# Optimization experiments

Hardware: AMD Instinct MI355X
Metric: run time of the kernel (lower is better)

Reference implementation:

```python
import jax, jax.numpy as jnp
import numpy as np

N = 50000      # nodes
E = 800000     # edges
HID = 64       # hidden_dim
HEADS = 4
DH = HID // HEADS
PIN = 128      # person_in_dim
DIN = 64       # disease_in_dim
NEXP = 4       # num_experts
K = 2          # topk
L = 2          # n_layers
NEG = 0.2      # gat_neg_slope


def setup_inputs() -> dict:
    key = jax.random.key(0)
    ks = iter(jax.random.split(key, 64))
    nrm = lambda shp, s=0.05: jax.random.normal(next(ks), shp, jnp.float32) * s
    d = {}
    d["features"] = jax.random.normal(next(ks), (N, PIN), jnp.float32)
    d["node_types"] = jax.random.randint(next(ks), (N,), 0, 2)
    d["src"] = jax.random.randint(next(ks), (E,), 0, N)
    d["dst"] = jax.random.randint(next(ks), (E,), 0, N)
    d["W_person"] = nrm((PIN, HID)); d["b_person"] = jnp.zeros((HID,), jnp.float32)
    d["W_disease"] = nrm((DIN, HID)); d["b_disease"] = jnp.zeros((HID,), jnp.float32)
    d["gat_W"] = nrm((L, HID, HID)); d["gat_al"] = nrm((L, HEADS, DH)); d["gat_ar"] = nrm((L, HEADS, DH))
    d["gin_eps"] = jnp.zeros((L,), jnp.float32)
    d["gin_W1"] = nrm((L, HID, HID)); d["gin_b1"] = jnp.zeros((L, HID), jnp.float32)
    d["gin_W2"] = nrm((L, HID, HID)); d["gin_b2"] = jnp.zeros((L, HID), jnp.float32)
    for p in ("gat", "gin"):
        d[p + "_gW"] = nrm((HID, NEXP)); d[p + "_gb"] = jnp.zeros((NEXP,), jnp.float32)
        d[p + "_eW1"] = nrm((NEXP, HID, HID // 2)); d[p + "_eb1"] = jnp.zeros((NEXP, HID // 2), jnp.float32)
        d[p + "_eW2"] = nrm((NEXP, HID // 2, HID)); d[p + "_eb2"] = jnp.zeros((NEXP, HID), jnp.float32)
    d["fg_W1"] = nrm((2 * HID, HID)); d["fg_b1"] = jnp.zeros((HID,), jnp.float32)
    d["fg_W2"] = nrm((HID, HID)); d["fg_b2"] = jnp.zeros((HID,), jnp.float32)
    return d


def _edge_softmax(logits, dst):
    m = jax.ops.segment_max(logits, dst, num_segments=N)
    e = jnp.exp(logits - m[dst])
    s = jax.ops.segment_sum(e, dst, num_segments=N)
    return e / (s[dst] + 1e-9)


def _gat(h, src, dst, gat_W, gat_al, gat_ar):
    for l in range(L):
        hW = (h @ gat_W[l]).reshape(N, HEADS, DH)
        el = (hW * gat_al[l]).sum(-1)                    # [N, HEADS]
        er = (hW * gat_ar[l]).sum(-1)
        lg = jax.nn.leaky_relu(el[src] + er[dst], NEG)   # [E, HEADS]
        a = _edge_softmax(lg, dst)
        out = jax.ops.segment_sum(hW[src] * a[:, :, None], dst, num_segments=N)
        h2 = out.reshape(N, HID) + h                     # residual=True
        h = jax.nn.relu(h2) if l < L - 1 else h2
    return h


def _gin(h, src, dst, gin_eps, gin_W1, gin_b1, gin_W2, gin_b2):
    deg = jax.ops.segment_sum(jnp.ones((E,), jnp.float32), dst, num_segments=N)
    inv = 1.0 / jnp.maximum(deg, 1.0)
    for l in range(L):
        agg = jax.ops.segment_sum(h[src], dst, num_segments=N) * inv[:, None]  # 'mean' aggregator
        x = (1.0 + gin_eps[l]) * h + agg                 # learn_eps=True
        x = jax.nn.relu(x @ gin_W1[l] + gin_b1[l]) @ gin_W2[l] + gin_b2[l]     # 2-layer MLP
        h = jax.nn.relu(x) if l < L - 1 else x
    return h


def _expert(h, gW, gb, eW1, eb1, eW2, eb2):
    probs = jax.nn.softmax(h @ gW + gb, axis=-1)         # [N, NEXP]
    topv, topi = jax.lax.top_k(probs, K)
    topv = topv / topv.sum(-1, keepdims=True)
    hot = jax.nn.one_hot(topi, NEXP, dtype=h.dtype)      # [N, K, NEXP]
    w = (hot * topv[..., None]).sum(1)                   # [N, NEXP] sparse weights
    e1 = jax.nn.relu(jnp.einsum('nd,edh->neh', h, eW1) + eb1)
    e2 = jnp.einsum('neh,ehd->ned', e1, eW2) + eb2       # [N, NEXP, HID]
    out = (e2 * w[:, :, None]).sum(1)
    f = hot.sum(1).mean(0)                               # routed fraction per expert
    P = probs.mean(0)
    aux = NEXP * jnp.sum(f * P)                          # switch-style load balancing
    return out, aux


def reference(features, node_types, src, dst, W_person, b_person, W_disease, b_disease,
              gat_W, gat_al, gat_ar, gin_eps, gin_W1, gin_b1, gin_W2, gin_b2,
              gat_gW, gat_gb, gat_eW1, gat_eb1, gat_eW2, gat_eb2,
              gin_gW, gin_gb, gin_eW1, gin_eb1, gin_eW2, gin_eb2,
              fg_W1, fg_b1, fg_W2, fg_b2):
    # per-type projection + scatter into shared buffer
    hp = features[:, :PIN] @ W_person + b_person
    hd = features[:, :DIN] @ W_disease + b_disease
    h = jnp.where((node_types == 0)[:, None], hp, hd)
    z_gat = _gat(h, src, dst, gat_W, gat_al, gat_ar)
    z_gin = _gin(h, src, dst, gin_eps, gin_W1, gin_b1, gin_W2, gin_b2)
    zg, aux_g = _expert(z_gat, gat_gW, gat_gb, gat_eW1, gat_eb1, gat_eW2, gat_eb2)
    zi, aux_i = _expert(z_gin, gin_gW, gin_gb, gin_eW1, gin_eb1, gin_eW2, gin_eb2)
    z = zi * zg
    u = jnp.concatenate([zg, zi], axis=-1)
    gate = jax.nn.sigmoid(jax.nn.relu(u @ fg_W1 + fg_b1) @ fg_W2 + fg_b2)
    u_prime = gate  # source calls fusion_gate(u) twice -> identical deterministic value
    z = gate * z + (1.0 - gate) * u_prime
    return z, aux_i + aux_g
```

## Files before the change

### kernel.cpp

```cpp
#include <hip/hip_runtime.h>

#define NN 50000
#define EE 800000
#define NEG 0.2f
#define NBG 391
#define NBT 392
#define NBKT 391
#define EPB 4096
#define NSEG 196

typedef __attribute__((ext_vector_type(8))) short s8;
typedef __attribute__((ext_vector_type(4))) float f4;

__device__ __forceinline__ float leaky(float x) { return x > 0.f ? x : NEG * x; }
__device__ __forceinline__ unsigned bf16r(float x) {
    unsigned u = __float_as_uint(x);
    return (u + 0x7fffu + ((u >> 16) & 1u)) >> 16;
}
__device__ __forceinline__ float lo16(unsigned p) { return __uint_as_float(p << 16); }
__device__ __forceinline__ float hi16(unsigned p) { return __uint_as_float(p & 0xffff0000u); }

__device__ __forceinline__ s8 a_from_f32(const float* p) {
    float4 u = *reinterpret_cast<const float4*>(p);
    float4 v = *reinterpret_cast<const float4*>(p + 4);
    s8 r;
    r[0] = (short)bf16r(u.x); r[1] = (short)bf16r(u.y);
    r[2] = (short)bf16r(u.z); r[3] = (short)bf16r(u.w);
    r[4] = (short)bf16r(v.x); r[5] = (short)bf16r(v.y);
    r[6] = (short)bf16r(v.z); r[7] = (short)bf16r(v.w);
    return r;
}

__global__ __launch_bounds__(256) void k_binA_pre(
        const int* __restrict__ src, const int* __restrict__ dst,
        int* __restrict__ seg_off, int* __restrict__ seg_cnt,
        unsigned* __restrict__ gseg, int* __restrict__ bucket_tot,
        const float* __restrict__ feat, const int* __restrict__ types,
        const float* __restrict__ Wp, const float* __restrict__ bp,
        const float* __restrict__ Wd, const float* __restrict__ bd,
        const float* __restrict__ gW, const float* __restrict__ al,
        const float* __restrict__ ar,
        float* __restrict__ h0f, unsigned* __restrict__ P,
        float* __restrict__ el, float* __restrict__ er) {
    __shared__ unsigned short WpT[64 * 136];
    __shared__ unsigned short WdT[64 * 72];
    __shared__ unsigned short WgT[64 * 72];
    __shared__ unsigned short y0s[4][16 * 72];
    if (blockIdx.x < NSEG) {
        unsigned* sbuf = (unsigned*)WpT;
        int* cnt = (int*)WdT;
        int* pre = (int*)WgT;
        int* ssc = (int*)y0s;
        for (int i = threadIdx.x; i < NBKT; i += 256) cnt[i] = 0;
        __syncthreads();
        int e0 = blockIdx.x * EPB;
        int nE = EE - e0; if (nE > EPB) nE = EPB;
        int b[16]; unsigned val[16]; int rk[16];
        #pragma unroll
        for (int i = 0; i < 16; i++) {
            int li = i * 256 + threadIdx.x;
            if (li < nE) {
                int e = e0 + li;
                int d = dst[e], s = src[e];
                b[i] = d >> 7;
                val[i] = ((unsigned)s << 7) | (unsigned)(d & 127);
                rk[i] = atomicAdd(&cnt[b[i]], 1);
            } else b[i] = -1;
        }
        __syncthreads();
        int t = threadIdx.x;
        int c0 = (2 * t     < NBKT) ? cnt[2 * t]     : 0;
        int c1 = (2 * t + 1 < NBKT) ? cnt[2 * t + 1] : 0;
        ssc[t] = c0 + c1;
        __syncthreads();
        for (int off = 1; off < 256; off <<= 1) {
            int u = (t >= off) ? ssc[t - off] : 0;
            __syncthreads();
            ssc[t] += u;
            __syncthreads();
        }
        int base = ssc[t] - (c0 + c1);
        pre[2 * t] = base;
        pre[2 * t + 1] = base + c0;
        __syncthreads();
        #pragma unroll
        for (int i = 0; i < 16; i++)
            if (b[i] >= 0) sbuf[pre[b[i]] + rk[i]] = val[i];
        for (int i = t; i < NBKT; i += 256) {
            seg_off[blockIdx.x * NBKT + i] = pre[i];
            seg_cnt[blockIdx.x * NBKT + i] = cnt[i];
            atomicAdd(&bucket_tot[i], cnt[i]);
        }
        __syncthreads();
        for (int i = t; i < nE; i += 256)
            gseg[(size_t)blockIdx.x * EPB + i] = sbuf[i];
        return;
    }
    for (int idx = threadIdx.x; idx < 128 * 64; idx += 256) {
        int k = idx >> 6, n = idx & 63;
        WpT[n * 136 + k] = (unsigned short)bf16r(Wp[idx]);
    }
    for (int idx = threadIdx.x; idx < 64 * 64; idx += 256) {
        int k = idx >> 6, n = idx & 63;
        WdT[n * 72 + k] = (unsigned short)bf16r(Wd[idx]);
        WgT[n * 72 + k] = (unsigned short)bf16r(gW[idx]);
    }
    __syncthreads();
    int wv = threadIdx.x >> 6, lane = threadIdx.x & 63;
    int quad = lane >> 4, l16 = lane & 15;
    int gw2 = (blockIdx.x - NSEG) * 4 + wv;
    int mtEnd = gw2 * 2 + 2; if (mtEnd > 3125) mtEnd = 3125;
    for (int mt = gw2 * 2; mt < mtEnd; mt++) {
        int row0 = mt * 16;
        const float* arow = feat + (size_t)(row0 + l16) * 128;
        f4 accp[4], accd[4];
        #pragma unroll
        for (int t = 0; t < 4; t++) { accp[t] = f4{0.f,0.f,0.f,0.f}; accd[t] = f4{0.f,0.f,0.f,0.f}; }
        #pragma unroll
        for (int ks = 0; ks < 4; ks++) {
            s8 a = a_from_f32(arow + ks * 32 + quad * 8);
            #pragma unroll
            for (int t = 0; t < 4; t++) {
                s8 b = *(const s8*)&WpT[(t * 16 + l16) * 136 + ks * 32 + quad * 8];
                accp[t] = __builtin_amdgcn_mfma_f32_16x16x32_bf16(a, b, accp[t], 0, 0, 0);
                if (ks < 2) {
                    s8 bd_ = *(const s8*)&WdT[(t * 16 + l16) * 72 + ks * 32 + quad * 8];
                    accd[t] = __builtin_amdgcn_mfma_f32_16x16x32_bf16(a, bd_, accd[t], 0, 0, 0);
                }
            }
        }
        int ty[4];
        #pragma unroll
        for (int r = 0; r < 4; r++) ty[r] = types[row0 + quad * 4 + r];
        float vv[4][4];
        #pragma unroll
        for (int t = 0; t < 4; t++) {
            int col = t * 16 + l16;
            float bpv = bp[col], bdv = bd[col];
            #pragma unroll
            for (int r = 0; r < 4; r++) {
                float v = ty[r] ? (accd[t][r] + bdv) : (accp[t][r] + bpv);
                vv[t][r] = v;
                h0f[(size_t)(row0 + quad * 4 + r) * 64 + col] = v;
                y0s[wv][(quad * 4 + r) * 72 + col] = (unsigned short)bf16r(v);
            }
        }
        s8 a0 = *(const s8*)&y0s[wv][l16 * 72 + quad * 8];
        s8 a1 = *(const s8*)&y0s[wv][l16 * 72 + 32 + quad * 8];
        f4 hw[4];
        #pragma unroll
        for (int t = 0; t < 4; t++) {
            hw[t] = f4{0.f,0.f,0.f,0.f};
            s8 b0 = *(const s8*)&WgT[(t * 16 + l16) * 72 + quad * 8];
            hw[t] = __builtin_amdgcn_mfma_f32_16x16x32_bf16(a0, b0, hw[t], 0, 0, 0);
            s8 b1_ = *(const s8*)&WgT[(t * 16 + l16) * 72 + 32 + quad * 8];
            hw[t] = __builtin_amdgcn_mfma_f32_16x16x32_bf16(a1, b1_, hw[t], 0, 0, 0);
        }
        #pragma unroll
        for (int t = 0; t < 4; t++) {
            int col = t * 16 + l16;
            float alv = al[col], arv = ar[col];
            #pragma unroll
            for (int r = 0; r < 4; r++) {
                int row = row0 + quad * 4 + r;
                float h = hw[t][r];
                P[(size_t)row * 64 + col] = bf16r(h) | (bf16r(vv[t][r]) << 16);
                float pl = h * alv, pr = h * arv;
                #pragma unroll
                for (int m = 1; m < 16; m <<= 1) {
                    pl += __shfl_xor(pl, m, 64);
                    pr += __shfl_xor(pr, m, 64);
                }
                if (l16 == 0) {
                    el[(size_t)row * 4 + t] = pl;
                    er[(size_t)row * 4 + t] = pr;
                }
            }
        }
    }
}

__global__ __launch_bounds__(256) void k_binB(
        int* __restrict__ row_start, const int* __restrict__ seg_off,
        const int* __restrict__ seg_cnt, const unsigned* __restrict__ gseg,
        int* __restrict__ csr_src, const int* __restrict__ bucket_tot) {
    __shared__ int spre[256];
    __shared__ int soff[NSEG];
    __shared__ int ss[256];
    __shared__ int kur[128];
    __shared__ int sred[4];
    int b = blockIdx.x;
    int t = threadIdx.x;
    int bt = 0;
    for (int i = t; i < b; i += 256) bt += bucket_tot[i];
    #pragma unroll
    for (int o2 = 1; o2 < 64; o2 <<= 1) bt += __shfl_xor(bt, o2, 64);
    if ((t & 63) == 0) sred[t >> 6] = bt;
    int c0 = (t < NSEG) ? seg_cnt[t * NBKT + b] : 0;
    if (t < NSEG) soff[t] = seg_off[t * NBKT + b];
    ss[t] = c0;
    __syncthreads();
    int bstart = sred[0] + sred[1] + sred[2] + sred[3];
    for (int off = 1; off < 256; off <<= 1) {
        int u = (t >= off) ? ss[t - off] : 0;
        __syncthreads();
        ss[t] += u;
        __syncthreads();
    }
    spre[t] = ss[t] - c0;
    int cntb = ss[255];
    if (t < 128) kur[t] = 0;
    __syncthreads();
    for (int idx = t; idx < cntb; idx += 256) {
        int lo = 0, hi = 255;
        #pragma unroll
        for (int s = 0; s < 8; s++) {
            int mid = (lo + hi + 1) >> 1;
            if (spre[mid] <= idx) lo = mid; else hi = mid - 1;
        }
        unsigned v = gseg[(size_t)lo * EPB + soff[lo] + (idx - spre[lo])];
        atomicAdd(&kur[v & 127], 1);
    }
    __syncthreads();
    int deg = (t < 128) ? kur[t] : 0;
    ss[t] = deg;
    __syncthreads();
    for (int off = 1; off < 256; off <<= 1) {
        int u = (t >= off) ? ss[t - off] : 0;
        __syncthreads();
        ss[t] += u;
        __syncthreads();
    }
    if (t < 128) {
        int cur = bstart + ss[t] - deg;
        kur[t] = cur;
        int d = (b << 7) + t;
        if (d < NN) row_start[d] = cur;
    }
    if (b == 0 && t == 0) row_start[NN] = EE;
    __syncthreads();
    for (int idx = t; idx < cntb; idx += 256) {
        int lo = 0, hi = 255;
        #pragma unroll
        for (int s = 0; s < 8; s++) {
            int mid = (lo + hi + 1) >> 1;
            if (spre[mid] <= idx) lo = mid; else hi = mid - 1;
        }
        unsigned v = gseg[(size_t)lo * EPB + soff[lo] + (idx - spre[lo])];
        int p = atomicAdd(&kur[v & 127], 1);
        csr_src[p] = (int)(v >> 7);
    }
}

template <int RELU>
__global__ void k_edges(const int* __restrict__ rows, const int* __restrict__ csr,
                        const unsigned* __restrict__ Pin,
                        const float* __restrict__ el, const float* __restrict__ er,
                        const float* __restrict__ gat_in, const float* __restrict__ gin_in,
                        const float* __restrict__ eps_p,
                        float* __restrict__ vgf, unsigned short* __restrict__ vgb,
                        unsigned short* __restrict__ xb) {
    __shared__ float ews[4][256];
    int wv = threadIdx.x >> 6, lane = threadIdx.x & 63;
    int n = blockIdx.x * 4 + wv;
    int st = rows[n], dg = rows[n + 1] - st;
    int hd = lane >> 4;
    float4 erv = *reinterpret_cast<const float4*>(er + (size_t)n * 4);
    float accg = 0.f, acci = 0.f, ssum = 0.f;
    for (int base = 0; base < dg; base += 64) {
        int rem = dg - base; if (rem > 64) rem = 64;
        int myi = 0;
        if (lane < rem) {
            myi = csr[st + base + lane];
            float4 lv = *reinterpret_cast<const float4*>(el + (size_t)myi * 4);
            float4 ev;
            ev.x = __expf(leaky(lv.x + erv.x));
            ev.y = __expf(leaky(lv.y + erv.y));
            ev.z = __expf(leaky(lv.z + erv.z));
            ev.w = __expf(leaky(lv.w + erv.w));
            *reinterpret_cast<float4*>(&ews[wv][lane * 4]) = ev;
        }
        int j = 0;
        for (; j + 4 <= rem; j += 4) {
            int s0 = __shfl(myi, j, 64),     s1 = __shfl(myi, j + 1, 64);
            int s2 = __shfl(myi, j + 2, 64), s3 = __shfl(myi, j + 3, 64);
            unsigned p0 = Pin[(size_t)s0 * 64 + lane];
            unsigned p1 = Pin[(size_t)s1 * 64 + lane];
            unsigned p2 = Pin[(size_t)s2 * 64 + lane];
            unsigned p3 = Pin[(size_t)s3 * 64 + lane];
            float a0 = ews[wv][(j + 0) * 4 + hd];
            float a1 = ews[wv][(j + 1) * 4 + hd];
            float a2 = ews[wv][(j + 2) * 4 + hd];
            float a3 = ews[wv][(j + 3) * 4 + hd];
            accg += a0 * lo16(p0) + a1 * lo16(p1) + a2 * lo16(p2) + a3 * lo16(p3);
            acci += hi16(p0) + hi16(p1) + hi16(p2) + hi16(p3);
            ssum += a0 + a1 + a2 + a3;
        }
        for (; j < rem; j++) {
            int s0 = __shfl(myi, j, 64);
            unsigned p0 = Pin[(size_t)s0 * 64 + lane];
            float a0 = ews[wv][j * 4 + hd];
            accg += a0 * lo16(p0); acci += hi16(p0); ssum += a0;
        }
    }
    float vg = accg / (ssum + 1e-9f) + gat_in[(size_t)n * 64 + lane];
    if (RELU) vg = fmaxf(vg, 0.f);
    float invd = 1.0f / fmaxf((float)dg, 1.0f);
    float x = (1.0f + eps_p[0]) * gin_in[(size_t)n * 64 + lane] + acci * invd;
    size_t off = (size_t)n * 64 + lane;
    vgf[off] = vg;
    vgb[off] = (unsigned short)bf16r(vg);
    xb[off] = (unsigned short)bf16r(x);
}

template <int L>
__global__ __launch_bounds__(256) void k_mlp(const unsigned short* __restrict__ Gx,
        const unsigned short* __restrict__ Eb,
        const float* __restrict__ W1, const float* __restrict__ b1,
        const float* __restrict__ W2, const float* __restrict__ b2,
        const float* __restrict__ gatW, const float* __restrict__ al,
        const float* __restrict__ ar,
        unsigned short* __restrict__ Fb, float* __restrict__ Cf,
        unsigned* __restrict__ P, float* __restrict__ el, float* __restrict__ er,
        const float* __restrict__ Zg, const float* __restrict__ ggW,
        const float* __restrict__ ggb, const float* __restrict__ igW,
        const float* __restrict__ igb,
        float* __restrict__ wgtg, float* __restrict__ wgti,
        float* __restrict__ stats) {
    __shared__ unsigned short W1T[64 * 72];
    __shared__ unsigned short W2T[64 * 72];
    __shared__ unsigned short WgT[(L == 0) ? 64 * 72 : 64];
    __shared__ unsigned short y1s[4][16 * 72];
    __shared__ float sstat[16];
    if (L == 1 && threadIdx.x < 16) sstat[threadIdx.x] = 0.f;
    for (int idx = threadIdx.x; idx < 64 * 64; idx += 256) {
        int k = idx >> 6, n = idx & 63;
        W1T[n * 72 + k] = (unsigned short)bf16r(W1[idx]);
        W2T[n * 72 + k] = (unsigned short)bf16r(W2[idx]);
        if (L == 0) WgT[n * 72 + k] = (unsigned short)bf16r(gatW[idx]);
    }
    __syncthreads();
    int wv = threadIdx.x >> 6, lane = threadIdx.x & 63;
    int quad = lane >> 4, l16 = lane & 15;
    int gw = blockIdx.x * 4 + wv;
    int mtEnd = gw * 2 + 2; if (mtEnd > 3125) mtEnd = 3125;
    float sp[2][4] = {{0,0,0,0},{0,0,0,0}};
    float sh[2][4] = {{0,0,0,0},{0,0,0,0}};
    for (int mt = gw * 2; mt < mtEnd; mt++) {
        int row0 = mt * 16;
        const unsigned short* arow = Gx + (size_t)(row0 + l16) * 64;
        s8 a0 = *(const s8*)(arow + quad * 8);
        s8 a1 = *(const s8*)(arow + 32 + quad * 8);
        f4 acc1[4];
        #pragma unroll
        for (int t = 0; t < 4; t++) {
            acc1[t] = f4{0.f,0.f,0.f,0.f};
            s8 b0 = *(const s8*)&W1T[(t * 16 + l16) * 72 + quad * 8];
            acc1[t] = __builtin_amdgcn_mfma_f32_16x16x32_bf16(a0, b0, acc1[t], 0, 0, 0);
            s8 b1_ = *(const s8*)&W1T[(t * 16 + l16) * 72 + 32 + quad * 8];
            acc1[t] = __builtin_amdgcn_mfma_f32_16x16x32_bf16(a1, b1_, acc1[t], 0, 0, 0);
        }
        #pragma unroll
        for (int t = 0; t < 4; t++) {
            float b1v = b1[t * 16 + l16];
            #pragma unroll
            for (int r = 0; r < 4; r++) {
                float v = fmaxf(acc1[t][r] + b1v, 0.f);
                y1s[wv][(quad * 4 + r) * 72 + t * 16 + l16] = (unsigned short)bf16r(v);
            }
        }
        s8 c0 = *(const s8*)&y1s[wv][l16 * 72 + quad * 8];
        s8 c1 = *(const s8*)&y1s[wv][l16 * 72 + 32 + quad * 8];
        f4 acc2[4];
        #pragma unroll
        for (int t = 0; t < 4; t++) {
            acc2[t] = f4{0.f,0.f,0.f,0.f};
            s8 b0 = *(const s8*)&W2T[(t * 16 + l16) * 72 + quad * 8];
            acc2[t] = __builtin_amdgcn_mfma_f32_16x16x32_bf16(c0, b0, acc2[t], 0, 0, 0);
            s8 b1_ = *(const s8*)&W2T[(t * 16 + l16) * 72 + 32 + quad * 8];
            acc2[t] = __builtin_amdgcn_mfma_f32_16x16x32_bf16(c1, b1_, acc2[t], 0, 0, 0);
        }
        unsigned short vb[4][4];
        float vout[4][4];
        #pragma unroll
        for (int t = 0; t < 4; t++) {
            int col = t * 16 + l16;
            float b2v = b2[col];
            #pragma unroll
            for (int r = 0; r < 4; r++) {
                float v = acc2[t][r] + b2v;
                if (L == 0) v = fmaxf(v, 0.f);
                size_t off = (size_t)(row0 + quad * 4 + r) * 64 + col;
                unsigned short vb16 = (unsigned short)bf16r(v);
                vb[t][r] = vb16;
                vout[t][r] = v;
                Fb[off] = vb16;
                if (L == 0) Cf[off] = v;
            }
        }
        if (L == 0) {
            const unsigned short* erow = Eb + (size_t)(row0 + l16) * 64;
            s8 e0 = *(const s8*)(erow + quad * 8);
            s8 e1 = *(const s8*)(erow + 32 + quad * 8);
            f4 hw[4];
            #pragma unroll
            for (int t = 0; t < 4; t++) {
                hw[t] = f4{0.f,0.f,0.f,0.f};
                s8 b0 = *(const s8*)&WgT[(t * 16 + l16) * 72 + quad * 8];
                hw[t] = __builtin_amdgcn_mfma_f32_16x16x32_bf16(e0, b0, hw[t], 0, 0, 0);
                s8 b1_ = *(const s8*)&WgT[(t * 16 + l16) * 72 + 32 + quad * 8];
                hw[t] = __builtin_amdgcn_mfma_f32_16x16x32_bf16(e1, b1_, hw[t], 0, 0, 0);
            }
            #pragma unroll
            for (int t = 0; t < 4; t++) {
                int col = t * 16 + l16;
                float alv = al[col], arv = ar[col];
                #pragma unroll
                for (int r = 0; r < 4; r++) {
                    int row = row0 + quad * 4 + r;
                    float h = hw[t][r];
                    P[(size_t)row * 64 + col] = bf16r(h) | ((unsigned)vb[t][r] << 16);
                    float pl = h * alv, pr = h * arv;
                    #pragma unroll
                    for (int m = 1; m < 16; m <<= 1) {
                        pl += __shfl_xor(pl, m, 64);
                        pr += __shfl_xor(pr, m, 64);
                    }
                    if (l16 == 0) {
                        el[(size_t)row * 4 + t] = pl;
                        er[(size_t)row * 4 + t] = pr;
                    }
                }
            }
        } else {
            #pragma unroll
            for (int r = 0; r < 4; r++) {
                int row = row0 + quad * 4 + r;
                float pg[4] = {0,0,0,0}, pi[4] = {0,0,0,0};
                #pragma unroll
                for (int t = 0; t < 4; t++) {
                    int col = t * 16 + l16;
                    float zgv = Zg[(size_t)row * 64 + col];
                    float ziv = vout[t][r];
                    #pragma unroll
                    for (int e = 0; e < 4; e++) {
                        pg[e] += zgv * ggW[col * 4 + e];
                        pi[e] += ziv * igW[col * 4 + e];
                    }
                }
                #pragma unroll
                for (int m = 1; m < 16; m <<= 1) {
                    #pragma unroll
                    for (int e = 0; e < 4; e++) {
                        pg[e] += __shfl_xor(pg[e], m, 64);
                        pi[e] += __shfl_xor(pi[e], m, 64);
                    }
                }
                if (l16 == 0) {
                    #pragma unroll
                    for (int q = 0; q < 2; q++) {
                        float lg0 = (q ? pi[0] + igb[0] : pg[0] + ggb[0]);
                        float lg1 = (q ? pi[1] + igb[1] : pg[1] + ggb[1]);
                        float lg2 = (q ? pi[2] + igb[2] : pg[2] + ggb[2]);
                        float lg3 = (q ? pi[3] + igb[3] : pg[3] + ggb[3]);
                        float mx = fmaxf(fmaxf(lg0, lg1), fmaxf(lg2, lg3));
                        float ex0 = __expf(lg0 - mx), ex1 = __expf(lg1 - mx);
                        float ex2 = __expf(lg2 - mx), ex3 = __expf(lg3 - mx);
                        float inv = 1.0f / (ex0 + ex1 + ex2 + ex3);
                        float pr4[4] = {ex0 * inv, ex1 * inv, ex2 * inv, ex3 * inv};
                        int i1 = 0; float v1 = pr4[0];
                        #pragma unroll
                        for (int t = 1; t < 4; t++) if (pr4[t] > v1) { v1 = pr4[t]; i1 = t; }
                        int i2 = -1; float v2 = -1.f;
                        #pragma unroll
                        for (int t = 0; t < 4; t++) if (t != i1 && pr4[t] > v2) { v2 = pr4[t]; i2 = t; }
                        float wsum = v1 + v2;
                        float wq[4] = {0.f, 0.f, 0.f, 0.f};
                        wq[i1] = v1 / wsum; wq[i2] = v2 / wsum;
                        float* WD = q ? wgti : wgtg;
                        *reinterpret_cast<float4*>(WD + (size_t)row * 4) =
                            float4{wq[0], wq[1], wq[2], wq[3]};
                        #pragma unroll
                        for (int t = 0; t < 4; t++) sp[q][t] += pr4[t];
                        sh[q][i1] += 1.f; sh[q][i2] += 1.f;
                    }
                }
            }
        }
    }
    if (L == 1) {
        __syncthreads();
        if (l16 == 0) {
            #pragma unroll
            for (int q = 0; q < 2; q++)
                #pragma unroll
                for (int e = 0; e < 4; e++) {
                    atomicAdd(&sstat[q * 8 + e], sp[q][e]);
                    atomicAdd(&sstat[q * 8 + 4 + e], sh[q][e]);
                }
        }
        __syncthreads();
        if (threadIdx.x < 16) atomicAdd(&stats[threadIdx.x], sstat[threadIdx.x]);
    }
}

__global__ __launch_bounds__(256) void k_tail(const unsigned short* __restrict__ Eb,
        const unsigned short* __restrict__ Fb,
        const float* __restrict__ g_eW1, const float* __restrict__ g_eb1,
        const float* __restrict__ g_eW2, const float* __restrict__ g_eb2,
        const float* __restrict__ i_eW1, const float* __restrict__ i_eb1,
        const float* __restrict__ i_eW2, const float* __restrict__ i_eb2,
        const float* __restrict__ wgtg, const float* __restrict__ wgti,
        const float* __restrict__ W1, const float* __restrict__ b1,
        const float* __restrict__ W2, const float* __restrict__ b2,
        unsigned short* __restrict__ ub, float* __restrict__ out,
        const float* __restrict__ stats) {
    __shared__ unsigned short wbuf[4 * 32 * 72 + 4 * 64 * 40];
    __shared__ unsigned short y1s[4][16 * 72];
    int wv = threadIdx.x >> 6, lane = threadIdx.x & 63;
    int quad = lane >> 4, l16 = lane & 15;
    int gw = blockIdx.x * 4 + wv;
    int mt0 = gw * 2;
    f4 moe[2][2][4];
    #pragma unroll
    for (int p = 0; p < 2; p++)
        #pragma unroll
        for (int m = 0; m < 2; m++)
            #pragma unroll
            for (int t = 0; t < 4; t++) moe[p][m][t] = f4{0.f,0.f,0.f,0.f};
    #pragma unroll
    for (int p = 0; p < 2; p++) {
        const unsigned short* Ab = p ? Fb : Eb;
        const float* eW1 = p ? i_eW1 : g_eW1;
        const float* eb1 = p ? i_eb1 : g_eb1;
        const float* eW2 = p ? i_eW2 : g_eW2;
        const float* eb2 = p ? i_eb2 : g_eb2;
        const float* wgt = p ? wgti : wgtg;
        int qoff = p ? 64 : 0;
        if (p) __syncthreads();
        for (int g = threadIdx.x; g < 8192; g += 256) {
            int e = g >> 11, rem = g & 2047;
            int k = rem >> 5, n = rem & 31;
            wbuf[e * 2304 + n * 72 + k] = (unsigned short)bf16r(eW1[g]);
        }
        for (int g = threadIdx.x; g < 8192; g += 256) {
            int e = g >> 11, rem = g & 2047;
            int k = rem >> 6, n = rem & 63;
            wbuf[9216 + e * 2560 + n * 40 + k] = (unsigned short)bf16r(eW2[g]);
        }
        __syncthreads();
        #pragma unroll
        for (int m = 0; m < 2; m++) {
            int mt = mt0 + m;
            if (mt < 3125) {
                int row0 = mt * 16;
                const unsigned short* arow = Ab + (size_t)(row0 + l16) * 64;
                s8 a0 = *(const s8*)(arow + quad * 8);
                s8 a1 = *(const s8*)(arow + 32 + quad * 8);
                for (int e = 0; e < 4; e++) {
                    f4 acc1[2];
                    #pragma unroll
                    for (int t = 0; t < 2; t++) {
                        acc1[t] = f4{0.f,0.f,0.f,0.f};
                        s8 b0 = *(const s8*)&wbuf[e * 2304 + (t * 16 + l16) * 72 + quad * 8];
                        acc1[t] = __builtin_amdgcn_mfma_f32_16x16x32_bf16(a0, b0, acc1[t], 0, 0, 0);
                        s8 b1_ = *(const s8*)&wbuf[e * 2304 + (t * 16 + l16) * 72 + 32 + quad * 8];
                        acc1[t] = __builtin_amdgcn_mfma_f32_16x16x32_bf16(a1, b1_, acc1[t], 0, 0, 0);
                    }
                    #pragma unroll
                    for (int t = 0; t < 2; t++) {
                        float b1v = eb1[e * 32 + t * 16 + l16];
                        #pragma unroll
                        for (int r = 0; r < 4; r++) {
                            float v = fmaxf(acc1[t][r] + b1v, 0.f);
                            y1s[wv][(quad * 4 + r) * 40 + t * 16 + l16] = (unsigned short)bf16r(v);
                        }
                    }
                    s8 a2 = *(const s8*)&y1s[wv][l16 * 40 + quad * 8];
                    f4 acc2[4];
                    #pragma unroll
                    for (int t = 0; t < 4; t++) {
                        acc2[t] = f4{0.f,0.f,0.f,0.f};
                        s8 b2_ = *(const s8*)&wbuf[9216 + e * 2560 + (t * 16 + l16) * 40 + quad * 8];
                        acc2[t] = __builtin_amdgcn_mfma_f32_16x16x32_bf16(a2, b2_, acc2[t], 0, 0, 0);
                    }
                    #pragma unroll
                    for (int t = 0; t < 4; t++) {
                        float b2v = eb2[e * 64 + t * 16 + l16];
                        #pragma unroll
                        for (int r = 0; r < 4; r++) {
                            float we = wgt[(size_t)(row0 + quad * 4 + r) * 4 + e];
                            moe[p][m][t][r] += we * (acc2[t][r] + b2v);
                        }
                    }
                }
                #pragma unroll
                for (int t = 0; t < 4; t++) {
                    int col = t * 16 + l16;
                    #pragma unroll
                    for (int r = 0; r < 4; r++) {
                        int row = row0 + quad * 4 + r;
                        ub[(size_t)row * 128 + qoff + col] = (unsigned short)bf16r(moe[p][m][t][r]);
                    }
                }
            }
        }
    }
    __syncthreads();
    for (int idx = threadIdx.x; idx < 128 * 64; idx += 256) {
        int k = idx >> 6, n = idx & 63;
        wbuf[n * 136 + k] = (unsigned short)bf16r(W1[idx]);
    }
    for (int idx = threadIdx.x; idx < 64 * 64; idx += 256) {
        int k = idx >> 6, n = idx & 63;
        wbuf[8704 + n * 72 + k] = (unsigned short)bf16r(W2[idx]);
    }
    __syncthreads();
    #pragma unroll
    for (int m = 0; m < 2; m++) {
        int mt = mt0 + m;
        if (mt < 3125) {
            int row0 = mt * 16;
            const unsigned short* arow = ub + (size_t)(row0 + l16) * 128;
            f4 acc1[4];
            #pragma unroll
            for (int t = 0; t < 4; t++) acc1[t] = f4{0.f,0.f,0.f,0.f};
            #pragma unroll
            for (int ks = 0; ks < 4; ks++) {
                s8 a = *(const s8*)(arow + ks * 32 + quad * 8);
                #pragma unroll
                for (int t = 0; t < 4; t++) {
                    s8 b = *(const s8*)&wbuf[(t * 16 + l16) * 136 + ks * 32 + quad * 8];
                    acc1[t] = __builtin_amdgcn_mfma_f32_16x16x32_bf16(a, b, acc1[t], 0, 0, 0);
                }
            }
            #pragma unroll
            for (int t = 0; t < 4; t++) {
                float b1v = b1[t * 16 + l16];
                #pragma unroll
                for (int r = 0; r < 4; r++) {
                    float v = fmaxf(acc1[t][r] + b1v, 0.f);
                    y1s[wv][(quad * 4 + r) * 72 + t * 16 + l16] = (unsigned short)bf16r(v);
                }
            }
            f4 acc2[4];
            #pragma unroll
            for (int t = 0; t < 4; t++) acc2[t] = f4{0.f,0.f,0.f,0.f};
            #pragma unroll
            for (int ks = 0; ks < 2; ks++) {
                s8 a = *(const s8*)&y1s[wv][l16 * 72 + ks * 32 + quad * 8];
                #pragma unroll
                for (int t = 0; t < 4; t++) {
                    s8 b = *(const s8*)&wbuf[8704 + (t * 16 + l16) * 72 + ks * 32 + quad * 8];
                    acc2[t] = __builtin_amdgcn_mfma_f32_16x16x32_bf16(a, b, acc2[t], 0, 0, 0);
                }
            }
            #pragma unroll
            for (int t = 0; t < 4; t++) {
                int col = t * 16 + l16;
                float b2v = b2[col];
                #pragma unroll
                for (int r = 0; r < 4; r++) {
                    int row = row0 + quad * 4 + r;
                    float g = 1.0f / (1.0f + __expf(-(acc2[t][r] + b2v)));
                    float zgv = moe[0][m][t][r];
                    float ziv = moe[1][m][t][r];
                    out[(size_t)row * 64 + col] = g * zgv * ziv + (1.0f - g) * g;
                }
            }
        }
    }
    if (blockIdx.x == 0 && threadIdx.x < 64) {
        int t = threadIdx.x;
        float s = (t < 16) ? stats[t] : 0.f;
        float aux = 0.f;
        for (int q = 0; q < 2; q++) {
            float a = 0.f;
            for (int e = 0; e < 4; e++) {
                float pr = __shfl(s, q * 8 + e, 64);
                float f  = __shfl(s, q * 8 + 4 + e, 64);
                a += (f / (float)NN) * (pr / (float)NN);
            }
            aux += 4.0f * a;
        }
        if (t == 0) out[(size_t)NN * 64] = aux;
    }
}

extern "C" void kernel_launch(void* const* d_in, const int* in_sizes, int n_in,
                              void* d_out, int out_size, void* d_ws, size_t ws_size,
                              hipStream_t stream) {
    (void)in_sizes; (void)n_in; (void)out_size; (void)ws_size;
    const float* features  = (const float*)d_in[0];
    const int*   node_types= (const int*)d_in[1];
    const int*   src       = (const int*)d_in[2];
    const int*   dst       = (const int*)d_in[3];
    const float* W_person  = (const float*)d_in[4];
    const float* b_person  = (const float*)d_in[5];
    const float* W_disease = (const float*)d_in[6];
    const float* b_disease = (const float*)d_in[7];
    const float* gat_W     = (const float*)d_in[8];
    const float* gat_al    = (const float*)d_in[9];
    const float* gat_ar    = (const float*)d_in[10];
    const float* gin_eps   = (const float*)d_in[11];
    const float* gin_W1    = (const float*)d_in[12];
    const float* gin_b1    = (const float*)d_in[13];
    const float* gin_W2    = (const float*)d_in[14];
    const float* gin_b2    = (const float*)d_in[15];
    const float* gat_gW    = (const float*)d_in[16];
    const float* gat_gb    = (const float*)d_in[17];
    const float* gat_eW1   = (const float*)d_in[18];
    const float* gat_eb1   = (const float*)d_in[19];
    const float* gat_eW2   = (const float*)d_in[20];
    const float* gat_eb2   = (const float*)d_in[21];
    const float* gin_gW    = (const float*)d_in[22];
    const float* gin_gb    = (const float*)d_in[23];
    const float* gin_eW1   = (const float*)d_in[24];
    const float* gin_eb1   = (const float*)d_in[25];
    const float* gin_eW2   = (const float*)d_in[26];
    const float* gin_eb2   = (const float*)d_in[27];
    const float* fg_W1     = (const float*)d_in[28];
    const float* fg_b1     = (const float*)d_in[29];
    const float* fg_W2     = (const float*)d_in[30];
    const float* fg_b2     = (const float*)d_in[31];
    float* out = (float*)d_out;

    float* ws = (float*)d_ws;
    size_t o = 0;
    float* A = ws + o; o += (size_t)NN * 64;
    float* B = ws + o; o += (size_t)NN * 64;
    float* C = ws + o; o += (size_t)NN * 64;
    unsigned short* E  = (unsigned short*)(ws + o); o += (size_t)NN * 32;
    unsigned short* F  = (unsigned short*)(ws + o); o += (size_t)NN * 32;
    unsigned short* G  = (unsigned short*)(ws + o); o += (size_t)NN * 32;
    unsigned* P = (unsigned*)(ws + o); o += (size_t)NN * 64;
    float* el = ws + o; o += (size_t)NN * 4;
    float* er = ws + o; o += (size_t)NN * 4;
    float* wgtg = ws + o; o += (size_t)NN * 4;
    float* wgti = ws + o; o += (size_t)NN * 4;
    int* bucket_tot = (int*)(ws + o); o += 392;
    float* stats    = ws + o; o += 16;
    int* row_start = (int*)(ws + o); o += NN + 4;
    int* csr_src   = (int*)(ws + o); o += EE;
    int* seg_off   = (int*)(ws + o); o += NSEG * NBKT + 64;
    int* seg_cnt   = (int*)(ws + o); o += NSEG * NBKT + 64;
    unsigned* gseg = (unsigned*)(ws + o); o += (size_t)NSEG * EPB;

    unsigned short* ub = (unsigned short*)A;

    const int NB_node = NN / 4;

    hipMemsetAsync(bucket_tot, 0, sizeof(int) * 392 + sizeof(float) * 16, stream);

    k_binA_pre<<<NSEG + NBG, 256, 0, stream>>>(src, dst, seg_off, seg_cnt, gseg, bucket_tot,
                                               features, node_types, W_person, b_person,
                                               W_disease, b_disease, gat_W, gat_al, gat_ar,
                                               A, P, el, er);

    k_binB<<<NBKT, 256, 0, stream>>>(row_start, seg_off, seg_cnt, gseg, csr_src, bucket_tot);

    k_edges<1><<<NB_node, 256, 0, stream>>>(row_start, csr_src, P, el, er, A, A,
                                            gin_eps, B, E, G);
    k_mlp<0><<<NBG, 256, 0, stream>>>(G, E, gin_W1, gin_b1, gin_W2, gin_b2,
                                      gat_W + 4096, gat_al + 64, gat_ar + 64,
                                      F, C, P, el, er,
                                      nullptr, nullptr, nullptr, nullptr, nullptr,
                                      nullptr, nullptr, nullptr);

    k_edges<0><<<NB_node, 256, 0, stream>>>(row_start, csr_src, P, el, er, B, C,
                                            gin_eps + 1, B, E, G);
    k_mlp<1><<<NBG, 256, 0, stream>>>(G, nullptr, gin_W1 + 4096, gin_b1 + 64,
                                      gin_W2 + 4096, gin_b2 + 64,
                                      nullptr, nullptr, nullptr,
                                      F, nullptr, nullptr, nullptr, nullptr,
                                      B, gat_gW, gat_gb, gin_gW, gin_gb,
                                      wgtg, wgti, stats);

    k_tail<<<NBT, 256, 0, stream>>>(E, F,
                                    gat_eW1, gat_eb1, gat_eW2, gat_eb2,
                                    gin_eW1, gin_eb1, gin_eW2, gin_eb2,
                                    wgtg, wgti, fg_W1, fg_b1, fg_W2, fg_b2,
                                    ub, out, stats);
}
```

Measured before the change: 316.4 us.

## Fuse final GIN MLP and gating into expert tail kernel

Merges the layer-2 MLP/gating kernel into the tail kernel. The GIN output tile and top-k gate weights now stay in registers and shared memory instead of going through global buffers F, wgtg and wgti. The aux loss is computed by the last block to finish, tracked with a done counter, which removes the cross-kernel dependency on stats. The cost is one less launch and less global traffic, traded for more registers and shared memory in the tail kernel.

New measurement: 321.8 us. No clear change (+1.7%).

```diff
diff --git a/kernel.cpp b/kernel.cpp
--- a/kernel.cpp
+++ b/kernel.cpp
@@ -313,39 +313,29 @@
     xb[off] = (unsigned short)bf16r(x);
 }
 
-template <int L>
-__global__ __launch_bounds__(256) void k_mlp(const unsigned short* __restrict__ Gx,
+__global__ __launch_bounds__(256) void k_mlp0(const unsigned short* __restrict__ Gx,
         const unsigned short* __restrict__ Eb,
         const float* __restrict__ W1, const float* __restrict__ b1,
         const float* __restrict__ W2, const float* __restrict__ b2,
         const float* __restrict__ gatW, const float* __restrict__ al,
         const float* __restrict__ ar,
-        unsigned short* __restrict__ Fb, float* __restrict__ Cf,
-        unsigned* __restrict__ P, float* __restrict__ el, float* __restrict__ er,
-        const float* __restrict__ Zg, const float* __restrict__ ggW,
-        const float* __restrict__ ggb, const float* __restrict__ igW,
-        const float* __restrict__ igb,
-        float* __restrict__ wgtg, float* __restrict__ wgti,
-        float* __restrict__ stats) {
+        float* __restrict__ Cf,
+        unsigned* __restrict__ P, float* __restrict__ el, float* __restrict__ er) {
     __shared__ unsigned short W1T[64 * 72];
     __shared__ unsigned short W2T[64 * 72];
-    __shared__ unsigned short WgT[(L == 0) ? 64 * 72 : 64];
+    __shared__ unsigned short WgT[64 * 72];
     __shared__ unsigned short y1s[4][16 * 72];
-    __shared__ float sstat[16];
-    if (L == 1 && threadIdx.x < 16) sstat[threadIdx.x] = 0.f;
     for (int idx = threadIdx.x; idx < 64 * 64; idx += 256) {
         int k = idx >> 6, n = idx & 63;
         W1T[n * 72 + k] = (unsigned short)bf16r(W1[idx]);
         W2T[n * 72 + k] = (unsigned short)bf16r(W2[idx]);
-        if (L == 0) WgT[n * 72 + k] = (unsigned short)bf16r(gatW[idx]);
+        WgT[n * 72 + k] = (unsigned short)bf16r(gatW[idx]);
     }
     __syncthreads();
     int wv = threadIdx.x >> 6, lane = threadIdx.x & 63;
     int quad = lane >> 4, l16 = lane & 15;
     int gw = blockIdx.x * 4 + wv;
     int mtEnd = gw * 2 + 2; if (mtEnd > 3125) mtEnd = 3125;
-    float sp[2][4] = {{0,0,0,0},{0,0,0,0}};
-    float sh[2][4] = {{0,0,0,0},{0,0,0,0}};
     for (int mt = gw * 2; mt < mtEnd; mt++) {
         int row0 = mt * 16;
         const unsigned short* arow = Gx + (size_t)(row0 + l16) * 64;
@@ -381,58 +371,144 @@
             acc2[t] = __builtin_amdgcn_mfma_f32_16x16x32_bf16(c1, b1_, acc2[t], 0, 0, 0);
         }
         unsigned short vb[4][4];
-        float vout[4][4];
         #pragma unroll
         for (int t = 0; t < 4; t++) {
             int col = t * 16 + l16;
             float b2v = b2[col];
             #pragma unroll
             for (int r = 0; r < 4; r++) {
-                float v = acc2[t][r] + b2v;
-                if (L == 0) v = fmaxf(v, 0.f);
+                float v = fmaxf(acc2[t][r] + b2v, 0.f);
                 size_t off = (size_t)(row0 + quad * 4 + r) * 64 + col;
-                unsigned short vb16 = (unsigned short)bf16r(v);
-                vb[t][r] = vb16;
-                vout[t][r] = v;
-                Fb[off] = vb16;
-                if (L == 0) Cf[off] = v;
-            }
-        }
-        if (L == 0) {
-            const unsigned short* erow = Eb + (size_t)(row0 + l16) * 64;
-            s8 e0 = *(const s8*)(erow + quad * 8);
-            s8 e1 = *(const s8*)(erow + 32 + quad * 8);
-            f4 hw[4];
+                vb[t][r] = (unsigned short)bf16r(v);
+                Cf[off] = v;
+            }
+        }
+        const unsigned short* erow = Eb + (size_t)(row0 + l16) * 64;
+        s8 e0 = *(const s8*)(erow + quad * 8);
+        s8 e1 = *(const s8*)(erow + 32 + quad * 8);
+        f4 hw[4];
+        #pragma unroll
+        for (int t = 0; t < 4; t++) {
+            hw[t] = f4{0.f,0.f,0.f,0.f};
+            s8 b0 = *(const s8*)&WgT[(t * 16 + l16) * 72 + quad * 8];
+            hw[t] = __builtin_amdgcn_mfma_f32_16x16x32_bf16(e0, b0, hw[t], 0, 0, 0);
+            s8 b1_ = *(const s8*)&WgT[(t * 16 + l16) * 72 + 32 + quad * 8];
+            hw[t] = __builtin_amdgcn_mfma_f32_16x16x32_bf16(e1, b1_, hw[t], 0, 0, 0);
+        }
+        #pragma unroll
+        for (int t = 0; t < 4; t++) {
+            int col = t * 16 + l16;
+            float alv = al[col], arv = ar[col];
+            #pragma unroll
+            for (int r = 0; r < 4; r++) {
+                int row = row0 + quad * 4 + r;
+                float h = hw[t][r];
+                P[(size_t)row * 64 + col] = bf16r(h) | ((unsigned)vb[t][r] << 16);
+                float pl = h * alv, pr = h * arv;
+                #pragma unroll
+                for (int m = 1; m < 16; m <<= 1) {
+                    pl += __shfl_xor(pl, m, 64);
+                    pr += __shfl_xor(pr, m, 64);
+                }
+                if (l16 == 0) {
+                    el[(size_t)row * 4 + t] = pl;
+                    er[(size_t)row * 4 + t] = pr;
+                }
+            }
+        }
+    }
+}
+
+__global__ __launch_bounds__(256) void k_tail(
+        const unsigned short* __restrict__ Gx,
+        const unsigned short* __restrict__ Eb,
+        const float* __restrict__ Zg,
+        const float* __restrict__ mW1, const float* __restrict__ mb1,
+        const float* __restrict__ mW2, const float* __restrict__ mb2,
+        const float* __restrict__ ggW, const float* __restrict__ ggb,
+        const float* __restrict__ igW, const float* __restrict__ igb,
+        const float* __restrict__ g_eW1, const float* __restrict__ g_eb1,
+        const float* __restrict__ g_eW2, const float* __restrict__ g_eb2,
+        const float* __restrict__ i_eW1, const float* __restrict__ i_eb1,
+        const float* __restrict__ i_eW2, const float* __restrict__ i_eb2,
+        const float* __restrict__ W1, const float* __restrict__ b1,
+        const float* __restrict__ W2, const float* __restrict__ b2,
+        unsigned short* __restrict__ ub, float* __restrict__ out,
+        float* __restrict__ stats, unsigned* __restrict__ done) {
+    __shared__ unsigned short wbuf[4 * 32 * 72 + 4 * 64 * 40];
+    __shared__ unsigned short y1s[4][16 * 72];
+    __shared__ float wqs[4][2][32][4];
+    __shared__ float sstat[16];
+    if (threadIdx.x < 16) sstat[threadIdx.x] = 0.f;
+    for (int idx = threadIdx.x; idx < 64 * 64; idx += 256) {
+        int k = idx >> 6, n = idx & 63;
+        wbuf[n * 72 + k] = (unsigned short)bf16r(mW1[idx]);
+        wbuf[4608 + n * 72 + k] = (unsigned short)bf16r(mW2[idx]);
+    }
+    __syncthreads();
+    int wv = threadIdx.x >> 6, lane = threadIdx.x & 63;
+    int quad = lane >> 4, l16 = lane & 15;
+    int gw = blockIdx.x * 4 + wv;
+    int mt0 = gw * 2;
+    float sp[2][4] = {{0,0,0,0},{0,0,0,0}};
+    float sh[2][4] = {{0,0,0,0},{0,0,0,0}};
+    s8 ai0_0{}, ai1_0{}, ai0_1{}, ai1_1{};
+    #pragma unroll
+    for (int m = 0; m < 2; m++) {
+        int mt = mt0 + m;
+        if (mt < 3125) {
+            int row0 = mt * 16;
+            const unsigned short* arow = Gx + (size_t)(row0 + l16) * 64;
+            s8 a0 = *(const s8*)(arow + quad * 8);
+            s8 a1 = *(const s8*)(arow + 32 + quad * 8);
+            f4 acc1[4];
             #pragma unroll
             for (int t = 0; t < 4; t++) {
-                hw[t] = f4{0.f,0.f,0.f,0.f};
-                s8 b0 = *(const s8*)&WgT[(t * 16 + l16) * 72 + quad * 8];
-                hw[t] = __builtin_amdgcn_mfma_f32_16x16x32_bf16(e0, b0, hw[t], 0, 0, 0);
-                s8 b1_ = *(const s8*)&WgT[(t * 16 + l16) * 72 + 32 + quad * 8];
-                hw[t] = __builtin_amdgcn_mfma_f32_16x16x32_bf16(e1, b1_, hw[t], 0, 0, 0);
+                acc1[t] = f4{0.f,0.f,0.f,0.f};
+                s8 b0 = *(const s8*)&wbuf[(t * 16 + l16) * 72 + quad * 8];
+                acc1[t] = __builtin_amdgcn_mfma_f32_16x16x32_bf16(a0, b0, acc1[t], 0, 0, 0);
+                s8 b1_ = *(const s8*)&wbuf[(t * 16 + l16) * 72 + 32 + quad * 8];
+                acc1[t] = __builtin_amdgcn_mfma_f32_16x16x32_bf16(a1, b1_, acc1[t], 0, 0, 0);
             }
             #pragma unroll
             for (int t = 0; t < 4; t++) {
-                int col = t * 16 + l16;
-                float alv = al[col], arv = ar[col];
+                float b1v = mb1[t * 16 + l16];
                 #pragma unroll
                 for (int r = 0; r < 4; r++) {
-                    int row = row0 + quad * 4 + r;
-                    float h = hw[t][r];
-                    P[(size_t)row * 64 + col] = bf16r(h) | ((unsigned)vb[t][r] << 16);
-                    float pl = h * alv, pr = h * arv;
-                    #pragma unroll
-                    for (int m = 1; m < 16; m <<= 1) {
-                        pl += __shfl_xor(pl, m, 64);
-                        pr += __shfl_xor(pr, m, 64);
-                    }
-                    if (l16 == 0) {
-                        el[(size_t)row * 4 + t] = pl;
-                        er[(size_t)row * 4 + t] = pr;
-                    }
-                }
-            }
-        } else {
+                    float v = fmaxf(acc1[t][r] + b1v, 0.f);
+                    y1s[wv][(quad * 4 + r) * 72 + t * 16 + l16] = (unsigned short)bf16r(v);
+                }
+            }
+            s8 c0 = *(const s8*)&y1s[wv][l16 * 72 + quad * 8];
+            s8 c1 = *(const s8*)&y1s[wv][l16 * 72 + 32 + quad * 8];
+            f4 acc2[4];
+            #pragma unroll
+            for (int t = 0; t < 4; t++) {
+                acc2[t] = f4{0.f,0.f,0.f,0.f};
+                s8 b0 = *(const s8*)&wbuf[4608 + (t * 16 + l16) * 72 + quad * 8];
+                acc2[t] = __builtin_amdgcn_mfma_f32_16x16x32_bf16(c0, b0, acc2[t], 0, 0, 0);
+                s8 b1_ = *(const s8*)&wbuf[4608 + (t * 16 + l16) * 72 + 32 + quad * 8];
+                acc2[t] = __builtin_amdgcn_mfma_f32_16x16x32_bf16(c1, b1_, acc2[t], 0, 0, 0);
+            }
+            float vout[4][4];
+            #pragma unroll
+            for (int t = 0; t < 4; t++) {
+                float b2v = mb2[t * 16 + l16];
+                #pragma unroll
+                for (int r = 0; r < 4; r++) vout[t][r] = acc2[t][r] + b2v;
+            }
+            #pragma unroll
+            for (int t = 0; t < 4; t++)
+                #pragma unroll
+                for (int r = 0; r < 4; r++)
+                    y1s[wv][(quad * 4 + r) * 72 + t * 16 + l16] = (unsigned short)bf16r(vout[t][r]);
+            if (m == 0) {
+                ai0_0 = *(const s8*)&y1s[wv][l16 * 72 + quad * 8];
+                ai1_0 = *(const s8*)&y1s[wv][l16 * 72 + 32 + quad * 8];
+            } else {
+                ai0_1 = *(const s8*)&y1s[wv][l16 * 72 + quad * 8];
+                ai1_1 = *(const s8*)&y1s[wv][l16 * 72 + 32 + quad * 8];
+            }
             #pragma unroll
             for (int r = 0; r < 4; r++) {
                 int row = row0 + quad * 4 + r;
@@ -449,11 +525,11 @@
                     }
                 }
                 #pragma unroll
-                for (int m = 1; m < 16; m <<= 1) {
+                for (int mm = 1; mm < 16; mm <<= 1) {
                     #pragma unroll
                     for (int e = 0; e < 4; e++) {
-                        pg[e] += __shfl_xor(pg[e], m, 64);
-                        pi[e] += __shfl_xor(pi[e], m, 64);
+                        pg[e] += __shfl_xor(pg[e], mm, 64);
+                        pi[e] += __shfl_xor(pi[e], mm, 64);
                     }
                 }
                 if (l16 == 0) {
@@ -477,9 +553,8 @@
                         float wsum = v1 + v2;
                         float wq[4] = {0.f, 0.f, 0.f, 0.f};
                         wq[i1] = v1 / wsum; wq[i2] = v2 / wsum;
-                        float* WD = q ? wgti : wgtg;
-                        *reinterpret_cast<float4*>(WD + (size_t)row * 4) =
-                            float4{wq[0], wq[1], wq[2], wq[3]};
+                        #pragma unroll
+                        for (int e = 0; e < 4; e++) wqs[wv][q][m * 16 + quad * 4 + r][e] = wq[e];
                         #pragma unroll
                         for (int t = 0; t < 4; t++) sp[q][t] += pr4[t];
                         sh[q][i1] += 1.f; sh[q][i2] += 1.f;
@@ -488,39 +563,35 @@
             }
         }
     }
-    if (L == 1) {
-        __syncthreads();
-        if (l16 == 0) {
-            #pragma unroll
-            for (int q = 0; q < 2; q++)
-                #pragma unroll
-                for (int e = 0; e < 4; e++) {
-                    atomicAdd(&sstat[q * 8 + e], sp[q][e]);
-                    atomicAdd(&sstat[q * 8 + 4 + e], sh[q][e]);
-                }
-        }
-        __syncthreads();
-        if (threadIdx.x < 16) atomicAdd(&stats[threadIdx.x], sstat[threadIdx.x]);
-    }
-}
-
-__global__ __launch_bounds__(256) void k_tail(const unsigned short* __restrict__ Eb,
-        const unsigned short* __restrict__ Fb,
-        const float* __restrict__ g_eW1, const float* __restrict__ g_eb1,
-        const float* __restrict__ g_eW2, const float* __restrict__ g_eb2,
-        const float* __restrict__ i_eW1, const float* __restrict__ i_eb1,
-        const float* __restrict__ i_eW2, const float* __restrict__ i_eb2,
-        const float* __restrict__ wgtg, const float* __restrict__ wgti,
-        const float* __restrict__ W1, const float* __restrict__ b1,
-        const float* __restrict__ W2, const float* __restrict__ b2,
-        unsigned short* __restrict__ ub, float* __restrict__ out,
-        const float* __restrict__ stats) {
-    __shared__ unsigned short wbuf[4 * 32 * 72 + 4 * 64 * 40];
-    __shared__ unsigned short y1s[4][16 * 72];
-    int wv = threadIdx.x >> 6, lane = threadIdx.x & 63;
-    int quad = lane >> 4, l16 = lane & 15;
-    int gw = blockIdx.x * 4 + wv;
-    int mt0 = gw * 2;
+    __syncthreads();
+    if (l16 == 0) {
+        #pragma unroll
+        for (int q = 0; q < 2; q++)
+            #pragma unroll
+            for (int e = 0; e < 4; e++) {
+                atomicAdd(&sstat[q * 8 + e], sp[q][e]);
+                atomicAdd(&sstat[q * 8 + 4 + e], sh[q][e]);
+            }
+    }
+    __syncthreads();
+    if (threadIdx.x < 16) atomicAdd(&stats[threadIdx.x], sstat[threadIdx.x]);
+    __syncthreads();
+    if (threadIdx.x == 0) {
+        unsigned rr = atomicAdd(done, 1u);
+        if (rr == (unsigned)(gridDim.x - 1)) {
+            float s[16];
+            #pragma unroll
+            for (int i = 0; i < 16; i++) s[i] = atomicAdd(&stats[i], 0.f);
+            float aux = 0.f;
+            for (int q = 0; q < 2; q++) {
+                float a = 0.f;
+                for (int e = 0; e < 4; e++)
+                    a += (s[q * 8 + 4 + e] / (float)NN) * (s[q * 8 + e] / (float)NN);
+                aux += 4.0f * a;
+            }
+            out[(size_t)NN * 64] = aux;
+        }
+    }
     f4 moe[2][2][4];
     #pragma unroll
     for (int p = 0; p < 2; p++)
@@ -530,12 +601,10 @@
             for (int t = 0; t < 4; t++) moe[p][m][t] = f4{0.f,0.f,0.f,0.f};
     #pragma unroll
     for (int p = 0; p < 2; p++) {
-        const unsigned short* Ab = p ? Fb : Eb;
         const float* eW1 = p ? i_eW1 : g_eW1;
         const float* eb1 = p ? i_eb1 : g_eb1;
         const float* eW2 = p ? i_eW2 : g_eW2;
         const float* eb2 = p ? i_eb2 : g_eb2;
-        const float* wgt = p ? wgti : wgtg;
         int qoff = p ? 64 : 0;
         if (p) __syncthreads();
         for (int g = threadIdx.x; g < 8192; g += 256) {
@@ -554,9 +623,15 @@
             int mt = mt0 + m;
             if (mt < 3125) {
                 int row0 = mt * 16;
-                const unsigned short* arow = Ab + (size_t)(row0 + l16) * 64;
-                s8 a0 = *(const s8*)(arow + quad * 8);
-                s8 a1 = *(const s8*)(arow + 32 + quad * 8);
+                s8 a0, a1;
+                if (p == 0) {
+                    const unsigned short* arow = Eb + (size_t)(row0 + l16) * 64;
+                    a0 = *(const s8*)(arow + quad * 8);
+                    a1 = *(const s8*)(arow + 32 + quad * 8);
+                } else {
+                    a0 = (m == 0) ? ai0_0 : ai0_1;
+                    a1 = (m == 0) ? ai1_0 : ai1_1;
+                }
                 for (int e = 0; e < 4; e++) {
                     f4 acc1[2];
                     #pragma unroll
@@ -589,7 +664,7 @@
                         float b2v = eb2[e * 64 + t * 16 + l16];
                         #pragma unroll
                         for (int r = 0; r < 4; r++) {
-                            float we = wgt[(size_t)(row0 + quad * 4 + r) * 4 + e];
+                            float we = wqs[wv][p][m * 16 + quad * 4 + r][e];
                             moe[p][m][t][r] += we * (acc2[t][r] + b2v);
                         }
                     }
@@ -669,21 +744,6 @@
                 }
             }
         }
-    }
-    if (blockIdx.x == 0 && threadIdx.x < 64) {
-        int t = threadIdx.x;
-        float s = (t < 16) ? stats[t] : 0.f;
-        float aux = 0.f;
-        for (int q = 0; q < 2; q++) {
-            float a = 0.f;
-            for (int e = 0; e < 4; e++) {
-                float pr = __shfl(s, q * 8 + e, 64);
-                float f  = __shfl(s, q * 8 + 4 + e, 64);
-                a += (f / (float)NN) * (pr / (float)NN);
-            }
-            aux += 4.0f * a;
-        }
-        if (t == 0) out[(size_t)NN * 64] = aux;
     }
 }
 
@@ -731,15 +791,13 @@
     float* B = ws + o; o += (size_t)NN * 64;
     float* C = ws + o; o += (size_t)NN * 64;
     unsigned short* E  = (unsigned short*)(ws + o); o += (size_t)NN * 32;
-    unsigned short* F  = (unsigned short*)(ws + o); o += (size_t)NN * 32;
     unsigned short* G  = (unsigned short*)(ws + o); o += (size_t)NN * 32;
     unsigned* P = (unsigned*)(ws + o); o += (size_t)NN * 64;
     float* el = ws + o; o += (size_t)NN * 4;
     float* er = ws + o; o += (size_t)NN * 4;
-    float* wgtg = ws + o; o += (size_t)NN * 4;
-    float* wgti = ws + o; o += (size_t)NN * 4;
     int* bucket_tot = (int*)(ws + o); o += 392;
     float* stats    = ws + o; o += 16;
+    unsigned* done  = (unsigned*)(ws + o); o += 4;
     int* row_start = (int*)(ws + o); o += NN + 4;
     int* csr_src   = (int*)(ws + o); o += EE;
     int* seg_off   = (int*)(ws + o); o += NSEG * NBKT + 64;
@@ -750,7 +808,7 @@
 
     const int NB_node = NN / 4;
 
-    hipMemsetAsync(bucket_tot, 0, sizeof(int) * 392 + sizeof(float) * 16, stream);
+    hipMemsetAsync(bucket_tot, 0, sizeof(int) * 392 + sizeof(float) * 16 + 16, stream);
 
     k_binA_pre<<<NSEG + NBG, 256, 0, stream>>>(src, dst, seg_off, seg_cnt, gseg, bucket_tot,
                                                features, node_types, W_person, b_person,
@@ -761,24 +819,18 @@
 
     k_edges<1><<<NB_node, 256, 0, stream>>>(row_start, csr_src, P, el, er, A, A,
                                             gin_eps, B, E, G);
-    k_mlp<0><<<NBG, 256, 0, stream>>>(G, E, gin_W1, gin_b1, gin_W2, gin_b2,
-                                      gat_W + 4096, gat_al + 64, gat_ar + 64,
-                                      F, C, P, el, er,
-                                      nullptr, nullptr, nullptr, nullptr, nullptr,
-                                      nullptr, nullptr, nullptr);
+    k_mlp0<<<NBG, 256, 0, stream>>>(G, E, gin_W1, gin_b1, gin_W2, gin_b2,
+                                    gat_W + 4096, gat_al + 64, gat_ar + 64,
+                                    C, P, el, er);
 
     k_edges<0><<<NB_node, 256, 0, stream>>>(row_start, csr_src, P, el, er, B, C,
                                             gin_eps + 1, B, E, G);
-    k_mlp<1><<<NBG, 256, 0, stream>>>(G, nullptr, gin_W1 + 4096, gin_b1 + 64,
-                                      gin_W2 + 4096, gin_b2 + 64,
-                                      nullptr, nullptr, nullptr,
-                                      F, nullptr, nullptr, nullptr, nullptr,
-                                      B, gat_gW, gat_gb, gin_gW, gin_gb,
-                                      wgtg, wgti, stats);
-
-    k_tail<<<NBT, 256, 0, stream>>>(E, F,
+
+    k_tail<<<NBT, 256, 0, stream>>>(G, E, B,
+                                    gin_W1 + 4096, gin_b1 + 64, gin_W2 + 4096, gin_b2 + 64,
+                                    gat_gW, gat_gb, gin_gW, gin_gb,
                                     gat_eW1, gat_eb1, gat_eW2, gat_eb2,
                                     gin_eW1, gin_eb1, gin_eW2, gin_eb2,
-                                    wgtg, wgti, fg_W1, fg_b1, fg_W2, fg_b2,
-                                    ub, out, stats);
+                                    fg_W1, fg_b1, fg_W2, fg_b2,
+                                    ub, out, stats, done);
 }
```
